# Kernel optimization log

Hardware: AMD Instinct MI355X
Metric: run time of the kernel (lower is better)

## Reference

```python
import jax, jax.numpy as jnp
import numpy as np
from jax import lax

D_MODEL = 1024
N_EXPERTS = 8
N_ACTIVE = 2
FFN_HIDDEN = int(D_MODEL * 2.0)


def setup_inputs() -> dict:
    key = jax.random.key(0)
    ks = jax.random.split(key, 7)
    B, T = 2, 2048
    s_in = 1.0 / np.sqrt(D_MODEL)
    s_h = 1.0 / np.sqrt(FFN_HIDDEN)
    return {
        "x": jax.random.normal(ks[0], (B, T, D_MODEL), dtype=jnp.float32),
        # router: torch Linear(d_model, n_experts, bias=False) weight [E, D]
        "router_w": jax.random.uniform(ks[1], (N_EXPERTS, D_MODEL), jnp.float32, -s_in, s_in),
        # stacked expert FFN params: w1 [E, H, D], b1 [E, H], w2 [E, D, H], b2 [E, D]
        "w1": jax.random.uniform(ks[2], (N_EXPERTS, FFN_HIDDEN, D_MODEL), jnp.float32, -s_in, s_in),
        "b1": jax.random.uniform(ks[3], (N_EXPERTS, FFN_HIDDEN), jnp.float32, -s_in, s_in),
        "w2": jax.random.uniform(ks[4], (N_EXPERTS, D_MODEL, FFN_HIDDEN), jnp.float32, -s_h, s_h),
        "b2": jax.random.uniform(ks[5], (N_EXPERTS, D_MODEL), jnp.float32, -s_h, s_h),
    }


def reference(x, router_w, w1, b1, w2, b2):
    B, T, D = x.shape
    N = B * T
    xf = x.reshape(N, D)

    logits = xf @ router_w.T                      # [N, E]
    probs = jax.nn.softmax(logits, axis=-1)       # [N, E]

    # --- aux load-balancing loss (f_i is non-differentiable, from indices) ---
    _, disp_idx = lax.top_k(logits, N_ACTIVE)     # [N, K]
    disp_mask = jax.nn.one_hot(disp_idx, N_EXPERTS, dtype=logits.dtype).sum(axis=1)  # [N, E]
    f_i = disp_mask.sum(axis=0) / (N * N_ACTIVE)  # [E]
    P_i = probs.mean(axis=0)                      # [E]
    aux_loss = N_EXPERTS * jnp.sum(f_i * P_i)

    # --- top-k combine weights, renormalized ---
    topk_w, topk_idx = lax.top_k(probs, N_ACTIVE)                 # [N, K]
    topk_w = topk_w / topk_w.sum(axis=-1, keepdims=True)
    # scatter top-k weights into dense [N, E] combine matrix (zeros elsewhere)
    combine_w = (jax.nn.one_hot(topk_idx, N_EXPERTS, dtype=xf.dtype) * topk_w[..., None]).sum(axis=1)

    # --- expert FFNs, weighted combine (loop over small fixed expert set) ---
    out = jnp.zeros_like(xf)
    for e in range(N_EXPERTS):
        h = jax.nn.silu(xf @ w1[e].T + b1[e])     # [N, H]
        y = h @ w2[e].T + b2[e]                   # [N, D]
        out = out + combine_w[:, e:e + 1] * y

    return out.reshape(B, T, D), aux_loss
```

## Files before the change

kernel.cpp:

```cpp
#include <hip/hip_runtime.h>
#include <cstdint>
#include <cstddef>

#define D_MODEL 1024
#define N_EXPERTS 8
#define FFN_H 2048
#define N_TOK 4096
#define CAP 2048

typedef float f32x4 __attribute__((ext_vector_type(4)));
typedef __bf16 bf16x8 __attribute__((ext_vector_type(8)));

static constexpr size_t XB_OFF   = 0;
static constexpr size_t W1B_OFF  = XB_OFF  + (size_t)N_TOK * D_MODEL * 2;
static constexpr size_t W2B_OFF  = W1B_OFF + (size_t)N_EXPERTS * FFN_H * D_MODEL * 2;
static constexpr size_t HBUF_OFF = W2B_OFF + (size_t)N_EXPERTS * D_MODEL * FFN_H * 2;
static constexpr size_t YBUF_OFF = HBUF_OFF + (size_t)N_EXPERTS * CAP * FFN_H * 2;
static constexpr size_t CNT_OFF  = YBUF_OFF + (size_t)N_EXPERTS * CAP * D_MODEL * 2;
static constexpr size_t PSUM_OFF = CNT_OFF + 32;
static constexpr size_t TOK_OFF  = PSUM_OFF + 32;
static constexpr size_t TIX_OFF  = TOK_OFF + (size_t)N_EXPERTS * CAP * 4;
static constexpr size_t TIW_OFF  = TIX_OFF + (size_t)N_TOK * 8;

__device__ __forceinline__ void async_ld16(const void* g, void* l) {
    __builtin_amdgcn_global_load_lds(
        (const __attribute__((address_space(1))) unsigned int*)g,
        (__attribute__((address_space(3))) unsigned int*)l, 16, 0, 0);
}

#define VMWAIT(n) asm volatile("s_waitcnt vmcnt(" #n ")" ::: "memory")
#define SBAR()    asm volatile("s_barrier" ::: "memory")

__global__ __launch_bounds__(256) void prep_kernel(const float* __restrict__ x,
                                                   const float* __restrict__ rw,
                                                   const float* __restrict__ w1,
                                                   const float* __restrict__ w2,
                                                   __bf16* __restrict__ xb,
                                                   __bf16* __restrict__ w1b,
                                                   __bf16* __restrict__ w2b,
                                                   int* __restrict__ counts,
                                                   float* __restrict__ psum,
                                                   int* __restrict__ tok_list,
                                                   int2* __restrict__ tinfo_idx,
                                                   float2* __restrict__ tinfo_w) {
    __shared__ float rws[N_EXPERTS * D_MODEL];
    __shared__ int s_e0[64], s_e1[64], s_r0[64], s_r1[64];
    __shared__ float s_w0[64], s_w1[64];
    __shared__ int hist[8], base[8];
    __shared__ float pacc[8];

    int tid = threadIdx.x;
    int b = blockIdx.x;
    if (b >= 64) {
        int c = b - 64;
        const float* src; __bf16* dst; size_t bb;
        if (c < 2048)       { src = x;  dst = xb;  bb = (size_t)c * 2048; }
        else if (c < 10240) { src = w1; dst = w1b; bb = (size_t)(c - 2048) * 2048; }
        else                { src = w2; dst = w2b; bb = (size_t)(c - 10240) * 2048; }
        size_t i = bb + (size_t)tid * 8;
        float4 a = *reinterpret_cast<const float4*>(src + i);
        float4 d = *reinterpret_cast<const float4*>(src + i + 4);
        bf16x8 r;
        r[0] = (__bf16)a.x; r[1] = (__bf16)a.y; r[2] = (__bf16)a.z; r[3] = (__bf16)a.w;
        r[4] = (__bf16)d.x; r[5] = (__bf16)d.y; r[6] = (__bf16)d.z; r[7] = (__bf16)d.w;
        *reinterpret_cast<bf16x8*>(dst + i) = r;
        return;
    }

    for (int i = tid * 4; i < N_EXPERTS * D_MODEL; i += 256 * 4)
        *reinterpret_cast<float4*>(&rws[i]) = *reinterpret_cast<const float4*>(&rw[i]);
    if (tid < 8) { hist[tid] = 0; pacc[tid] = 0.f; }
    __syncthreads();

    int wave = tid >> 6, lane = tid & 63;
    float psacc[8] = {};
    for (int it = 0; it < 16; ++it) {
        int li = wave * 16 + it;
        int t = b * 64 + li;
        const float* xr = x + (size_t)t * D_MODEL;
        float acc[8] = {};
#pragma unroll
        for (int i = 0; i < D_MODEL / 64; ++i) {
            float xv = xr[lane + 64 * i];
#pragma unroll
            for (int e = 0; e < 8; ++e) acc[e] += xv * rws[e * D_MODEL + lane + 64 * i];
        }
        float logit[8];
#pragma unroll
        for (int e = 0; e < 8; ++e) {
            float v = acc[e];
            for (int off = 32; off; off >>= 1) v += __shfl_xor(v, off);
            logit[e] = v;
        }
        float mx = logit[0];
#pragma unroll
        for (int e = 1; e < 8; ++e) mx = fmaxf(mx, logit[e]);
        float p[8], s = 0.f;
#pragma unroll
        for (int e = 0; e < 8; ++e) { p[e] = expf(logit[e] - mx); s += p[e]; }
        float inv = 1.f / s;
#pragma unroll
        for (int e = 0; e < 8; ++e) { p[e] *= inv; psacc[e] += p[e]; }
        int e0 = 0; float p0 = p[0];
#pragma unroll
        for (int e = 1; e < 8; ++e) if (p[e] > p0) { p0 = p[e]; e0 = e; }
        int e1 = -1; float p1 = -1.f;
#pragma unroll
        for (int e = 0; e < 8; ++e) if (e != e0 && p[e] > p1) { p1 = p[e]; e1 = e; }
        float invw = 1.f / (p0 + p1);
        if (lane == 0) {
            s_e0[li] = e0; s_e1[li] = e1;
            s_w0[li] = p0 * invw; s_w1[li] = p1 * invw;
        }
    }
    if (lane == 0)
#pragma unroll
        for (int e = 0; e < 8; ++e) atomicAdd(&pacc[e], psacc[e]);
    __syncthreads();

    if (tid < 64) {
        s_r0[tid] = atomicAdd(&hist[s_e0[tid]], 1);
        s_r1[tid] = atomicAdd(&hist[s_e1[tid]], 1);
    }
    __syncthreads();
    if (tid < 8) {
        base[tid] = atomicAdd(&counts[tid], hist[tid]);
        atomicAdd(&psum[tid], pacc[tid]);
    }
    __syncthreads();
    if (tid < 64) {
        int t = b * 64 + tid;
        int e0 = s_e0[tid], e1 = s_e1[tid];
        int q0 = min(base[e0] + s_r0[tid], CAP - 1);
        int q1 = min(base[e1] + s_r1[tid], CAP - 1);
        tok_list[e0 * CAP + q0] = t;
        tok_list[e1 * CAP + q1] = t;
        tinfo_idx[t] = make_int2(e0 * CAP + q0, e1 * CAP + q1);
        tinfo_w[t] = make_float2(s_w0[tid], s_w1[tid]);
    }
}

template <int KDIM, bool PASS2>
__global__ __launch_bounds__(256, 2) void ffn_kernel(const __bf16* __restrict__ A_base,
                                                     const __bf16* __restrict__ B_base,
                                                     const float* __restrict__ bias,
                                                     const int* __restrict__ counts,
                                                     const int* __restrict__ tok_list,
                                                     __bf16* __restrict__ Out_base) {
    constexpr int BROWS = PASS2 ? D_MODEL : FFN_H;
    constexpr int NT = BROWS / 128;
    constexpr int NSTEP = KDIM / 32;
    int bid = blockIdx.x;
    int e = bid & 7;
    int r = bid >> 3;
    int n0 = (r % NT) * 128;
    int m0 = (r / NT) * 128;
    int cnt = min(counts[e], CAP);
    if (m0 >= cnt) return;

    __shared__ char smem[65536];

    int tid = threadIdx.x;
    int* s_tok = (int*)smem;
    if (!PASS2 && tid < 128) {
        int slot = min(m0 + tid, cnt - 1);
        s_tok[tid] = tok_list[e * CAP + slot];
    }
    __syncthreads();

    int colk = ((tid & 3) ^ ((tid >> 3) & 3)) * 8;
    const __bf16 *a_src0, *a_src1;
    if (PASS2) {
        int s0 = min(m0 + (tid >> 2), cnt - 1);
        int s1 = min(m0 + 64 + (tid >> 2), cnt - 1);
        a_src0 = A_base + ((size_t)e * CAP + s0) * KDIM + colk;
        a_src1 = A_base + ((size_t)e * CAP + s1) * KDIM + colk;
    } else {
        a_src0 = A_base + (size_t)s_tok[tid >> 2] * KDIM + colk;
        a_src1 = A_base + (size_t)s_tok[64 + (tid >> 2)] * KDIM + colk;
    }
    const __bf16* b_src0 = B_base + ((size_t)e * BROWS + n0 + (tid >> 2)) * KDIM + colk;
    const __bf16* b_src1 = b_src0 + (size_t)64 * KDIM;
    __syncthreads();

    int wv = tid >> 6, lane = tid & 63;
    int wm = wv >> 1, wn = wv & 1;
    int lm = lane & 15, q = lane >> 4;
    int rsw = (q ^ ((lm >> 1) & 3)) * 8;
    int a_base = (wm * 64 + lm) * 32 + rsw;
    int b_base = (wn * 64 + lm) * 32 + rsw;
    int wofs = (tid >> 6) * 1024;

    float bv[4];
    {
        int nb = e * BROWS + n0 + wn * 64 + lm;
#pragma unroll
        for (int fn = 0; fn < 4; ++fn) bv[fn] = bias[nb + fn * 16];
    }
    VMWAIT(0);

    f32x4 acc[4][4] = {};

    auto stage = [&](int t) {
        int k0 = t * 32;
        int b4 = (t & 3) * 8192;
        char* la = smem + b4 + wofs;
        char* lb = smem + 32768 + b4 + wofs;
        async_ld16(a_src0 + k0, la);
        async_ld16(a_src1 + k0, la + 4096);
        async_ld16(b_src0 + k0, lb);
        async_ld16(b_src1 + k0, lb + 4096);
    };
    auto compute = [&](int t) {
        int b4 = (t & 3) * 8192;
        const __bf16* pa = (const __bf16*)(smem + b4);
        const __bf16* pb = (const __bf16*)(smem + 32768 + b4);
        bf16x8 af[4], bfg[4];
#pragma unroll
        for (int f = 0; f < 4; ++f) {
            af[f]  = *reinterpret_cast<const bf16x8*>(&pa[a_base + f * 512]);
            bfg[f] = *reinterpret_cast<const bf16x8*>(&pb[b_base + f * 512]);
        }
        __builtin_amdgcn_s_setprio(1);
#pragma unroll
        for (int fm = 0; fm < 4; ++fm)
#pragma unroll
            for (int fn = 0; fn < 4; ++fn)
                acc[fm][fn] = __builtin_amdgcn_mfma_f32_16x16x32_bf16(af[fm], bfg[fn], acc[fm][fn], 0, 0, 0);
        __builtin_amdgcn_s_setprio(0);
    };

    stage(0); stage(1); stage(2);

    for (int t = 0; t < NSTEP - 3; ++t) {
        VMWAIT(8);
        SBAR();
        stage(t + 3);
        compute(t);
    }
    VMWAIT(8); SBAR(); compute(NSTEP - 3);
    VMWAIT(4); SBAR(); compute(NSTEP - 2);
    VMWAIT(0); SBAR(); compute(NSTEP - 1);
    __syncthreads();

    __bf16* ep = (__bf16*)(smem) + wv * (64 * 72);
#pragma unroll
    for (int fn = 0; fn < 4; ++fn) {
#pragma unroll
        for (int fm = 0; fm < 4; ++fm)
#pragma unroll
            for (int i = 0; i < 4; ++i) {
                float v = acc[fm][fn][i] + bv[fn];
                if (!PASS2) v = v / (1.f + __expf(-v));
                ep[(fm * 16 + q * 4 + i) * 72 + fn * 16 + lm] = (__bf16)v;
            }
    }
    __syncthreads();
    int rr = lane >> 3, ccol = (lane & 7) * 8;
#pragma unroll
    for (int rep = 0; rep < 8; ++rep) {
        int rw = rep * 8 + rr;
        int slot = m0 + wm * 64 + rw;
        bf16x8 vv = *reinterpret_cast<const bf16x8*>(&ep[rw * 72 + ccol]);
        if (slot < cnt)
            *reinterpret_cast<bf16x8*>(
                &Out_base[((size_t)e * CAP + slot) * BROWS + n0 + wn * 64 + ccol]) = vv;
    }
}

__global__ __launch_bounds__(256) void combine_kernel(const __bf16* __restrict__ ybuf,
                                                      const int2* __restrict__ tinfo_idx,
                                                      const float2* __restrict__ tinfo_w,
                                                      const int* __restrict__ counts,
                                                      const float* __restrict__ psum,
                                                      float* __restrict__ out) {
    int tid = threadIdx.x;
    if (blockIdx.x == 0 && tid == 0) {
        float s = 0.f;
#pragma unroll
        for (int e = 0; e < 8; ++e)
            s += ((float)counts[e] / (float)(N_TOK * 2)) * (psum[e] / (float)N_TOK);
        out[(size_t)N_TOK * D_MODEL] = 8.f * s;
    }
    int t = blockIdx.x * 2 + (tid >> 7);
    int d0 = (tid & 127) * 8;
    int2 ix = tinfo_idx[t];
    float2 w = tinfo_w[t];
    bf16x8 ya = *reinterpret_cast<const bf16x8*>(ybuf + (size_t)ix.x * D_MODEL + d0);
    bf16x8 yb = *reinterpret_cast<const bf16x8*>(ybuf + (size_t)ix.y * D_MODEL + d0);
    float4 o0, o1;
    o0.x = w.x * (float)ya[0] + w.y * (float)yb[0];
    o0.y = w.x * (float)ya[1] + w.y * (float)yb[1];
    o0.z = w.x * (float)ya[2] + w.y * (float)yb[2];
    o0.w = w.x * (float)ya[3] + w.y * (float)yb[3];
    o1.x = w.x * (float)ya[4] + w.y * (float)yb[4];
    o1.y = w.x * (float)ya[5] + w.y * (float)yb[5];
    o1.z = w.x * (float)ya[6] + w.y * (float)yb[6];
    o1.w = w.x * (float)ya[7] + w.y * (float)yb[7];
    float* op = out + (size_t)t * D_MODEL + d0;
    *reinterpret_cast<float4*>(op) = o0;
    *reinterpret_cast<float4*>(op + 4) = o1;
}

extern "C" void kernel_launch(void* const* d_in, const int* in_sizes, int n_in,
                              void* d_out, int out_size, void* d_ws, size_t ws_size,
                              hipStream_t stream) {
    const float* x  = (const float*)d_in[0];
    const float* rw = (const float*)d_in[1];
    const float* w1 = (const float*)d_in[2];
    const float* b1 = (const float*)d_in[3];
    const float* w2 = (const float*)d_in[4];
    const float* b2 = (const float*)d_in[5];
    float* out = (float*)d_out;

    char* ws = (char*)d_ws;
    __bf16* xb     = (__bf16*)(ws + XB_OFF);
    __bf16* w1b    = (__bf16*)(ws + W1B_OFF);
    __bf16* w2b    = (__bf16*)(ws + W2B_OFF);
    __bf16* hbuf   = (__bf16*)(ws + HBUF_OFF);
    __bf16* ybuf   = (__bf16*)(ws + YBUF_OFF);
    int*    counts = (int*)(ws + CNT_OFF);
    float*  psum   = (float*)(ws + PSUM_OFF);
    int*    tok    = (int*)(ws + TOK_OFF);
    int2*   tix    = (int2*)(ws + TIX_OFF);
    float2* tiw    = (float2*)(ws + TIW_OFF);

    hipMemsetAsync(ws + CNT_OFF, 0, 64, stream);

    prep_kernel<<<64 + 18432, 256, 0, stream>>>(x, rw, w1, w2, xb, w1b, w2b,
                                                counts, psum, tok, tix, tiw);

    ffn_kernel<D_MODEL, false><<<8 * (FFN_H / 128) * (CAP / 128), 256, 0, stream>>>(
        xb, w1b, b1, counts, tok, hbuf);
    ffn_kernel<FFN_H, true><<<8 * (D_MODEL / 128) * (CAP / 128), 256, 0, stream>>>(
        hbuf, w2b, b2, counts, tok, ybuf);

    combine_kernel<<<N_TOK / 2, 256, 0, stream>>>(ybuf, tix, tiw, counts, psum, out);
}
```

Baseline: 294.1 us.

## Fuse weight bf16 conversion into GEMM loads and scatter-add combine via atomics

The separate pass that converts w1/w2 to bf16 in workspace is removed. The FFN GEMMs now load fp32 weights through registers, convert them, and write bf16 into LDS, with the K step widened to 64 and double buffering in place of the 4-stage async pipeline. The combine kernel and the ybuf intermediate are dropped: pass 2 atomically adds weighted outputs into a zeroed fp32 output, and the aux loss moves into pass 2. This saves weight conversion traffic and a launch, but each GEMM block now reads fp32 weights (twice the bytes, reread by every M tile) and pays atomic contention and a weaker load pipeline.

```diff
diff --git a/kernel.cpp b/kernel.cpp
--- a/kernel.cpp
+++ b/kernel.cpp
@@ -12,15 +12,11 @@
 typedef __bf16 bf16x8 __attribute__((ext_vector_type(8)));
 
 static constexpr size_t XB_OFF   = 0;
-static constexpr size_t W1B_OFF  = XB_OFF  + (size_t)N_TOK * D_MODEL * 2;
-static constexpr size_t W2B_OFF  = W1B_OFF + (size_t)N_EXPERTS * FFN_H * D_MODEL * 2;
-static constexpr size_t HBUF_OFF = W2B_OFF + (size_t)N_EXPERTS * D_MODEL * FFN_H * 2;
-static constexpr size_t YBUF_OFF = HBUF_OFF + (size_t)N_EXPERTS * CAP * FFN_H * 2;
-static constexpr size_t CNT_OFF  = YBUF_OFF + (size_t)N_EXPERTS * CAP * D_MODEL * 2;
+static constexpr size_t HBUF_OFF = XB_OFF + (size_t)N_TOK * D_MODEL * 2;
+static constexpr size_t CNT_OFF  = HBUF_OFF + (size_t)N_EXPERTS * CAP * FFN_H * 2;
 static constexpr size_t PSUM_OFF = CNT_OFF + 32;
 static constexpr size_t TOK_OFF  = PSUM_OFF + 32;
-static constexpr size_t TIX_OFF  = TOK_OFF + (size_t)N_EXPERTS * CAP * 4;
-static constexpr size_t TIW_OFF  = TIX_OFF + (size_t)N_TOK * 8;
+static constexpr size_t WGT_OFF  = TOK_OFF + (size_t)N_EXPERTS * CAP * 4;
 
 __device__ __forceinline__ void async_ld16(const void* g, void* l) {
     __builtin_amdgcn_global_load_lds(
@@ -28,21 +24,21 @@
         (__attribute__((address_space(3))) unsigned int*)l, 16, 0, 0);
 }
 
-#define VMWAIT(n) asm volatile("s_waitcnt vmcnt(" #n ")" ::: "memory")
-#define SBAR()    asm volatile("s_barrier" ::: "memory")
+__device__ __forceinline__ bf16x8 cvt8(float4 lo, float4 hi) {
+    bf16x8 r;
+    r[0] = (__bf16)lo.x; r[1] = (__bf16)lo.y; r[2] = (__bf16)lo.z; r[3] = (__bf16)lo.w;
+    r[4] = (__bf16)hi.x; r[5] = (__bf16)hi.y; r[6] = (__bf16)hi.z; r[7] = (__bf16)hi.w;
+    return r;
+}
 
 __global__ __launch_bounds__(256) void prep_kernel(const float* __restrict__ x,
                                                    const float* __restrict__ rw,
-                                                   const float* __restrict__ w1,
-                                                   const float* __restrict__ w2,
                                                    __bf16* __restrict__ xb,
-                                                   __bf16* __restrict__ w1b,
-                                                   __bf16* __restrict__ w2b,
                                                    int* __restrict__ counts,
                                                    float* __restrict__ psum,
                                                    int* __restrict__ tok_list,
-                                                   int2* __restrict__ tinfo_idx,
-                                                   float2* __restrict__ tinfo_w) {
+                                                   float* __restrict__ wgt_list,
+                                                   float* __restrict__ out) {
     __shared__ float rws[N_EXPERTS * D_MODEL];
     __shared__ int s_e0[64], s_e1[64], s_r0[64], s_r1[64];
     __shared__ float s_w0[64], s_w1[64];
@@ -53,17 +49,16 @@
     int b = blockIdx.x;
     if (b >= 64) {
         int c = b - 64;
-        const float* src; __bf16* dst; size_t bb;
-        if (c < 2048)       { src = x;  dst = xb;  bb = (size_t)c * 2048; }
-        else if (c < 10240) { src = w1; dst = w1b; bb = (size_t)(c - 2048) * 2048; }
-        else                { src = w2; dst = w2b; bb = (size_t)(c - 10240) * 2048; }
-        size_t i = bb + (size_t)tid * 8;
-        float4 a = *reinterpret_cast<const float4*>(src + i);
-        float4 d = *reinterpret_cast<const float4*>(src + i + 4);
+        size_t i = (size_t)c * 2048 + (size_t)tid * 8;
+        float4 a = *reinterpret_cast<const float4*>(x + i);
+        float4 d = *reinterpret_cast<const float4*>(x + i + 4);
         bf16x8 r;
         r[0] = (__bf16)a.x; r[1] = (__bf16)a.y; r[2] = (__bf16)a.z; r[3] = (__bf16)a.w;
         r[4] = (__bf16)d.x; r[5] = (__bf16)d.y; r[6] = (__bf16)d.z; r[7] = (__bf16)d.w;
-        *reinterpret_cast<bf16x8*>(dst + i) = r;
+        *reinterpret_cast<bf16x8*>(xb + i) = r;
+        float4 z = {0.f, 0.f, 0.f, 0.f};
+        *reinterpret_cast<float4*>(out + i) = z;
+        *reinterpret_cast<float4*>(out + i + 4) = z;
         return;
     }
 
@@ -135,22 +130,35 @@
         int q1 = min(base[e1] + s_r1[tid], CAP - 1);
         tok_list[e0 * CAP + q0] = t;
         tok_list[e1 * CAP + q1] = t;
-        tinfo_idx[t] = make_int2(e0 * CAP + q0, e1 * CAP + q1);
-        tinfo_w[t] = make_float2(s_w0[tid], s_w1[tid]);
+        wgt_list[e0 * CAP + q0] = s_w0[tid];
+        wgt_list[e1 * CAP + q1] = s_w1[tid];
     }
 }
 
 template <int KDIM, bool PASS2>
 __global__ __launch_bounds__(256, 2) void ffn_kernel(const __bf16* __restrict__ A_base,
-                                                     const __bf16* __restrict__ B_base,
+                                                     const float* __restrict__ B_base,
                                                      const float* __restrict__ bias,
                                                      const int* __restrict__ counts,
                                                      const int* __restrict__ tok_list,
-                                                     __bf16* __restrict__ Out_base) {
+                                                     const float* __restrict__ wgt_list,
+                                                     const float* __restrict__ psum,
+                                                     __bf16* __restrict__ HOut,
+                                                     float* __restrict__ FOut) {
     constexpr int BROWS = PASS2 ? D_MODEL : FFN_H;
     constexpr int NT = BROWS / 128;
-    constexpr int NSTEP = KDIM / 32;
+    constexpr int NSTEP = KDIM / 64;
     int bid = blockIdx.x;
+    int tid = threadIdx.x;
+
+    if (PASS2 && bid == 0 && tid == 0) {
+        float s = 0.f;
+#pragma unroll
+        for (int e = 0; e < 8; ++e)
+            s += ((float)counts[e] / (float)(N_TOK * 2)) * (psum[e] / (float)N_TOK);
+        FOut[(size_t)N_TOK * D_MODEL] = 8.f * s;
+    }
+
     int e = bid & 7;
     int r = bid >> 3;
     int n0 = (r % NT) * 128;
@@ -160,7 +168,6 @@
 
     __shared__ char smem[65536];
 
-    int tid = threadIdx.x;
     int* s_tok = (int*)smem;
     if (!PASS2 && tid < 128) {
         int slot = min(m0 + tid, cnt - 1);
@@ -179,9 +186,13 @@
         a_src0 = A_base + (size_t)s_tok[tid >> 2] * KDIM + colk;
         a_src1 = A_base + (size_t)s_tok[64 + (tid >> 2)] * KDIM + colk;
     }
-    const __bf16* b_src0 = B_base + ((size_t)e * BROWS + n0 + (tid >> 2)) * KDIM + colk;
-    const __bf16* b_src1 = b_src0 + (size_t)64 * KDIM;
-    __syncthreads();
+    __syncthreads();
+
+    const float* w_src0 = B_base + ((size_t)e * BROWS + n0 + (tid >> 2)) * KDIM + (tid & 3) * 8;
+    const float* w_src1 = w_src0 + (size_t)64 * KDIM;
+    int swzcb  = ((tid & 3) ^ ((tid >> 3) & 3)) * 16;
+    int wr_off0 = (tid >> 2) * 64 + swzcb;
+    int wr_off1 = wr_off0 + 4096;
 
     int wv = tid >> 6, lane = tid & 63;
     int wm = wv >> 1, wn = wv & 1;
@@ -197,109 +208,105 @@
 #pragma unroll
         for (int fn = 0; fn < 4; ++fn) bv[fn] = bias[nb + fn * 16];
     }
-    VMWAIT(0);
 
     f32x4 acc[4][4] = {};
-
-    auto stage = [&](int t) {
-        int k0 = t * 32;
-        int b4 = (t & 3) * 8192;
-        char* la = smem + b4 + wofs;
-        char* lb = smem + 32768 + b4 + wofs;
-        async_ld16(a_src0 + k0, la);
-        async_ld16(a_src1 + k0, la + 4096);
-        async_ld16(b_src0 + k0, lb);
-        async_ld16(b_src1 + k0, lb + 4096);
+    float4 b00, b01, b02, b03, b10, b11, b12, b13;
+
+    auto stageA = [&](int t) {
+        int k0 = t * 64;
+        char* la = smem + (t & 1) * 16384 + wofs;
+        async_ld16(a_src0 + k0,      la);
+        async_ld16(a_src1 + k0,      la + 4096);
+        async_ld16(a_src0 + k0 + 32, la + 8192);
+        async_ld16(a_src1 + k0 + 32, la + 8192 + 4096);
     };
-    auto compute = [&](int t) {
-        int b4 = (t & 3) * 8192;
-        const __bf16* pa = (const __bf16*)(smem + b4);
-        const __bf16* pb = (const __bf16*)(smem + 32768 + b4);
-        bf16x8 af[4], bfg[4];
-#pragma unroll
-        for (int f = 0; f < 4; ++f) {
-            af[f]  = *reinterpret_cast<const bf16x8*>(&pa[a_base + f * 512]);
-            bfg[f] = *reinterpret_cast<const bf16x8*>(&pb[b_base + f * 512]);
-        }
-        __builtin_amdgcn_s_setprio(1);
+    auto loadB = [&](int t) {
+        int k0 = t * 64;
+        b00 = *reinterpret_cast<const float4*>(w_src0 + k0);
+        b01 = *reinterpret_cast<const float4*>(w_src0 + k0 + 4);
+        b02 = *reinterpret_cast<const float4*>(w_src0 + k0 + 32);
+        b03 = *reinterpret_cast<const float4*>(w_src0 + k0 + 36);
+        b10 = *reinterpret_cast<const float4*>(w_src1 + k0);
+        b11 = *reinterpret_cast<const float4*>(w_src1 + k0 + 4);
+        b12 = *reinterpret_cast<const float4*>(w_src1 + k0 + 32);
+        b13 = *reinterpret_cast<const float4*>(w_src1 + k0 + 36);
+    };
+    auto writeB = [&](int t) {
+        char* lb = smem + 32768 + (t & 1) * 16384;
+        *reinterpret_cast<bf16x8*>(lb + wr_off0)        = cvt8(b00, b01);
+        *reinterpret_cast<bf16x8*>(lb + 8192 + wr_off0) = cvt8(b02, b03);
+        *reinterpret_cast<bf16x8*>(lb + wr_off1)        = cvt8(b10, b11);
+        *reinterpret_cast<bf16x8*>(lb + 8192 + wr_off1) = cvt8(b12, b13);
+    };
+    auto compute = [&](int buf) {
+#pragma unroll
+        for (int kk = 0; kk < 2; ++kk) {
+            const __bf16* pa = (const __bf16*)(smem + (buf * 2 + kk) * 8192);
+            const __bf16* pb = (const __bf16*)(smem + 32768 + (buf * 2 + kk) * 8192);
+            bf16x8 af[4], bfg[4];
+#pragma unroll
+            for (int f = 0; f < 4; ++f) {
+                af[f]  = *reinterpret_cast<const bf16x8*>(&pa[a_base + f * 512]);
+                bfg[f] = *reinterpret_cast<const bf16x8*>(&pb[b_base + f * 512]);
+            }
+#pragma unroll
+            for (int fm = 0; fm < 4; ++fm)
+#pragma unroll
+                for (int fn = 0; fn < 4; ++fn)
+                    acc[fm][fn] = __builtin_amdgcn_mfma_f32_16x16x32_bf16(af[fm], bfg[fn], acc[fm][fn], 0, 0, 0);
+        }
+    };
+
+    stageA(0); loadB(0); writeB(0);
+    __syncthreads();
+
+    for (int t = 0; t < NSTEP; ++t) {
+        if (t + 1 < NSTEP) { stageA(t + 1); loadB(t + 1); }
+        compute(t & 1);
+        if (t + 1 < NSTEP) writeB(t + 1);
+        __syncthreads();
+    }
+
+    if (!PASS2) {
+        __bf16* ep = (__bf16*)(smem) + wv * (64 * 72);
+#pragma unroll
+        for (int fn = 0; fn < 4; ++fn) {
+#pragma unroll
+            for (int fm = 0; fm < 4; ++fm)
+#pragma unroll
+                for (int i = 0; i < 4; ++i) {
+                    float v = acc[fm][fn][i] + bv[fn];
+                    v = v / (1.f + __expf(-v));
+                    ep[(fm * 16 + q * 4 + i) * 72 + fn * 16 + lm] = (__bf16)v;
+                }
+        }
+        __syncthreads();
+        int rr = lane >> 3, ccol = (lane & 7) * 8;
+#pragma unroll
+        for (int rep = 0; rep < 8; ++rep) {
+            int rw = rep * 8 + rr;
+            int slot = m0 + wm * 64 + rw;
+            bf16x8 vv = *reinterpret_cast<const bf16x8*>(&ep[rw * 72 + ccol]);
+            if (slot < cnt)
+                *reinterpret_cast<bf16x8*>(
+                    &HOut[((size_t)e * CAP + slot) * FFN_H + n0 + wn * 64 + ccol]) = vv;
+        }
+    } else {
 #pragma unroll
         for (int fm = 0; fm < 4; ++fm)
 #pragma unroll
-            for (int fn = 0; fn < 4; ++fn)
-                acc[fm][fn] = __builtin_amdgcn_mfma_f32_16x16x32_bf16(af[fm], bfg[fn], acc[fm][fn], 0, 0, 0);
-        __builtin_amdgcn_s_setprio(0);
-    };
-
-    stage(0); stage(1); stage(2);
-
-    for (int t = 0; t < NSTEP - 3; ++t) {
-        VMWAIT(8);
-        SBAR();
-        stage(t + 3);
-        compute(t);
-    }
-    VMWAIT(8); SBAR(); compute(NSTEP - 3);
-    VMWAIT(4); SBAR(); compute(NSTEP - 2);
-    VMWAIT(0); SBAR(); compute(NSTEP - 1);
-    __syncthreads();
-
-    __bf16* ep = (__bf16*)(smem) + wv * (64 * 72);
-#pragma unroll
-    for (int fn = 0; fn < 4; ++fn) {
-#pragma unroll
-        for (int fm = 0; fm < 4; ++fm)
-#pragma unroll
             for (int i = 0; i < 4; ++i) {
-                float v = acc[fm][fn][i] + bv[fn];
-                if (!PASS2) v = v / (1.f + __expf(-v));
-                ep[(fm * 16 + q * 4 + i) * 72 + fn * 16 + lm] = (__bf16)v;
+                int slot = m0 + wm * 64 + fm * 16 + q * 4 + i;
+                if (slot < cnt) {
+                    int tok = tok_list[e * CAP + slot];
+                    float w = wgt_list[e * CAP + slot];
+                    float* op = FOut + (size_t)tok * D_MODEL + n0 + wn * 64 + lm;
+#pragma unroll
+                    for (int fn = 0; fn < 4; ++fn)
+                        atomicAdd(op + fn * 16, w * (acc[fm][fn][i] + bv[fn]));
+                }
             }
     }
-    __syncthreads();
-    int rr = lane >> 3, ccol = (lane & 7) * 8;
-#pragma unroll
-    for (int rep = 0; rep < 8; ++rep) {
-        int rw = rep * 8 + rr;
-        int slot = m0 + wm * 64 + rw;
-        bf16x8 vv = *reinterpret_cast<const bf16x8*>(&ep[rw * 72 + ccol]);
-        if (slot < cnt)
-            *reinterpret_cast<bf16x8*>(
-                &Out_base[((size_t)e * CAP + slot) * BROWS + n0 + wn * 64 + ccol]) = vv;
-    }
-}
-
-__global__ __launch_bounds__(256) void combine_kernel(const __bf16* __restrict__ ybuf,
-                                                      const int2* __restrict__ tinfo_idx,
-                                                      const float2* __restrict__ tinfo_w,
-                                                      const int* __restrict__ counts,
-                                                      const float* __restrict__ psum,
-                                                      float* __restrict__ out) {
-    int tid = threadIdx.x;
-    if (blockIdx.x == 0 && tid == 0) {
-        float s = 0.f;
-#pragma unroll
-        for (int e = 0; e < 8; ++e)
-            s += ((float)counts[e] / (float)(N_TOK * 2)) * (psum[e] / (float)N_TOK);
-        out[(size_t)N_TOK * D_MODEL] = 8.f * s;
-    }
-    int t = blockIdx.x * 2 + (tid >> 7);
-    int d0 = (tid & 127) * 8;
-    int2 ix = tinfo_idx[t];
-    float2 w = tinfo_w[t];
-    bf16x8 ya = *reinterpret_cast<const bf16x8*>(ybuf + (size_t)ix.x * D_MODEL + d0);
-    bf16x8 yb = *reinterpret_cast<const bf16x8*>(ybuf + (size_t)ix.y * D_MODEL + d0);
-    float4 o0, o1;
-    o0.x = w.x * (float)ya[0] + w.y * (float)yb[0];
-    o0.y = w.x * (float)ya[1] + w.y * (float)yb[1];
-    o0.z = w.x * (float)ya[2] + w.y * (float)yb[2];
-    o0.w = w.x * (float)ya[3] + w.y * (float)yb[3];
-    o1.x = w.x * (float)ya[4] + w.y * (float)yb[4];
-    o1.y = w.x * (float)ya[5] + w.y * (float)yb[5];
-    o1.z = w.x * (float)ya[6] + w.y * (float)yb[6];
-    o1.w = w.x * (float)ya[7] + w.y * (float)yb[7];
-    float* op = out + (size_t)t * D_MODEL + d0;
-    *reinterpret_cast<float4*>(op) = o0;
-    *reinterpret_cast<float4*>(op + 4) = o1;
 }
 
 extern "C" void kernel_launch(void* const* d_in, const int* in_sizes, int n_in,
@@ -315,25 +322,18 @@
 
     char* ws = (char*)d_ws;
     __bf16* xb     = (__bf16*)(ws + XB_OFF);
-    __bf16* w1b    = (__bf16*)(ws + W1B_OFF);
-    __bf16* w2b    = (__bf16*)(ws + W2B_OFF);
     __bf16* hbuf   = (__bf16*)(ws + HBUF_OFF);
-    __bf16* ybuf   = (__bf16*)(ws + YBUF_OFF);
     int*    counts = (int*)(ws + CNT_OFF);
     float*  psum   = (float*)(ws + PSUM_OFF);
     int*    tok    = (int*)(ws + TOK_OFF);
-    int2*   tix    = (int2*)(ws + TIX_OFF);
-    float2* tiw    = (float2*)(ws + TIW_OFF);
+    float*  wgt    = (float*)(ws + WGT_OFF);
 
     hipMemsetAsync(ws + CNT_OFF, 0, 64, stream);
 
-    prep_kernel<<<64 + 18432, 256, 0, stream>>>(x, rw, w1, w2, xb, w1b, w2b,
-                                                counts, psum, tok, tix, tiw);
+    prep_kernel<<<64 + 2048, 256, 0, stream>>>(x, rw, xb, counts, psum, tok, wgt, out);
 
     ffn_kernel<D_MODEL, false><<<8 * (FFN_H / 128) * (CAP / 128), 256, 0, stream>>>(
-        xb, w1b, b1, counts, tok, hbuf);
+        xb, w1, b1, counts, tok, nullptr, nullptr, hbuf, nullptr);
     ffn_kernel<FFN_H, true><<<8 * (D_MODEL / 128) * (CAP / 128), 256, 0, stream>>>(
-        hbuf, w2b, b2, counts, tok, ybuf);
-
-    combine_kernel<<<N_TOK / 2, 256, 0, stream>>>(ybuf, tix, tiw, counts, psum, out);
-}
+        hbuf, w2, b2, counts, tok, wgt, psum, nullptr, out);
+}
```

New measurement: 394.7 us. 34.2% more time.
